# Optimization experiments

Hardware: AMD Instinct MI355X
Metric: run time of the kernel (lower is better)

The kernel has to match this reference:

```python
import jax, jax.numpy as jnp
import numpy as np

N_NODES = 50000
N_EDGES = 800000


def setup_inputs() -> dict:
    key = jax.random.key(0)
    ks = jax.random.split(key, 12)
    x = jax.random.normal(ks[0], (N_NODES, 500), dtype=jnp.float32)
    edge_src = jax.random.randint(ks[1], (N_EDGES,), 0, N_NODES, dtype=jnp.int32)
    edge_dst = jax.random.randint(ks[2], (N_EDGES,), 0, N_NODES, dtype=jnp.int32)
    edge_vals = jax.random.uniform(ks[3], (N_EDGES,), dtype=jnp.float32) * 0.1
    def w(k, fan_in, fan_out):
        s = 1.0 / np.sqrt(fan_in)
        return jax.random.uniform(k, (fan_in, fan_out), dtype=jnp.float32, minval=-s, maxval=s)
    W1 = w(ks[4], 500, 128)
    b1 = jnp.zeros((128,), jnp.float32)
    W2 = w(ks[5], 128, 64)
    b2 = jnp.zeros((64,), jnp.float32)
    W3 = w(ks[6], 64, 16)
    b3 = jnp.zeros((16,), jnp.float32)
    We = w(ks[7], 64, 64)
    be = jnp.zeros((64,), jnp.float32)
    return {"x": x, "edge_vals": edge_vals, "W1": W1, "b1": b1, "W2": W2,
            "b2": b2, "W3": W3, "b3": b3, "We": We, "be": be,
            "edge_src": edge_src, "edge_dst": edge_dst}


def reference(x, edge_vals, W1, b1, W2, b2, W3, b3, We, be, edge_src, edge_dst):
    n = x.shape[0]

    def gcn_layer(h, W, b):
        # GraphConvolution: support = h @ W ; out = spmm(adj, support) + b
        support = h @ W                                   # [N, d_out]
        msg = support[edge_dst] * edge_vals[:, None]      # [E, d_out]
        agg = jax.ops.segment_sum(msg, edge_src, num_segments=n)
        return agg + b

    h = jax.nn.relu(gcn_layer(x, W1, b1))
    # dropout omitted (eval mode, training=False)
    h = jax.nn.relu(gcn_layer(h, W2, b2))
    out1 = jax.nn.log_softmax(gcn_layer(h, W3, b3), axis=1)
    out2 = h @ We + be
    return (out1, out2)
```

## Files before the change

### kernel.cpp

```cpp
#include <hip/hip_runtime.h>
#include <math.h>

#define N_NODES 50000
#define N_EDGES 800000

typedef __attribute__((ext_vector_type(8))) short bf16x8;
typedef __attribute__((ext_vector_type(4))) float f32x4;

__device__ inline unsigned short f2bf(float f) {
    unsigned u = __float_as_uint(f);
    unsigned r = (u + 0x7fffu + ((u >> 16) & 1u)) >> 16;
    return (unsigned short)r;
}

__global__ __launch_bounds__(256) void convert_w1_kernel(
    const float* __restrict__ W1, unsigned short* __restrict__ W1bf)
{
    int t = blockIdx.x * 256 + threadIdx.x;
    int n = t >> 9, k = t & 511;
    float v = (k < 500) ? W1[k * 128 + n] : 0.0f;
    W1bf[t] = f2bf(v);
}

__global__ __launch_bounds__(256) void gemm1_mfma_kernel(
    const float* __restrict__ A,
    const unsigned short* __restrict__ Bt,
    unsigned short* __restrict__ C)
{
    constexpr int K = 500, N = 128, BM = 64;
    constexpr int LDA = 56;
    __shared__ __align__(16) unsigned short As[BM * LDA];

    const int t = threadIdx.x;
    const int row0 = blockIdx.x * BM;
    const int lane = t & 63;
    const int wave = t >> 6;
    const int wm = (wave & 1) * 32;
    const int wn = (wave >> 1) * 64;
    const int l15 = lane & 15;
    const int l4  = lane >> 4;

    const int m0 = t >> 3, kq = t & 7;
    const int m1 = m0 + 32;
    const float* arow0 = A + (size_t)(row0 + m0) * K;
    const float* arow1 = A + (size_t)(row0 + m1) * K;
    const bool rv0 = (row0 + m0) < N_NODES;
    const bool rv1 = (row0 + m1) < N_NODES;

    const f32x4 zero = {0.0f, 0.0f, 0.0f, 0.0f};
    f32x4 acc[2][4];
#pragma unroll
    for (int i = 0; i < 2; ++i)
#pragma unroll
        for (int j = 0; j < 4; ++j) acc[i][j] = zero;

    float4 pf0, pf1;
    auto ldA = [&](int k0, float4& d, const float* row, bool rowok) {
        int k = k0 + kq * 4;
        if (rowok && k < K) d = *reinterpret_cast<const float4*>(row + k);
        else d = make_float4(0.0f, 0.0f, 0.0f, 0.0f);
    };
    ldA(0, pf0, arow0, rv0);
    ldA(0, pf1, arow1, rv1);

    for (int s = 0; s < 16; ++s) {
        const int k0 = s * 32;
        __syncthreads();
        {
            unsigned short h[4];
            h[0] = f2bf(pf0.x); h[1] = f2bf(pf0.y);
            h[2] = f2bf(pf0.z); h[3] = f2bf(pf0.w);
            *reinterpret_cast<uint2*>(&As[m0 * LDA + kq * 4]) =
                *reinterpret_cast<uint2*>(h);
            h[0] = f2bf(pf1.x); h[1] = f2bf(pf1.y);
            h[2] = f2bf(pf1.z); h[3] = f2bf(pf1.w);
            *reinterpret_cast<uint2*>(&As[m1 * LDA + kq * 4]) =
                *reinterpret_cast<uint2*>(h);
        }
        __syncthreads();
        if (s < 15) {
            ldA(k0 + 32, pf0, arow0, rv0);
            ldA(k0 + 32, pf1, arow1, rv1);
        }

        bf16x8 af[2];
#pragma unroll
        for (int i = 0; i < 2; ++i) {
            int m = wm + i * 16 + l15;
            af[i] = *reinterpret_cast<const bf16x8*>(&As[m * LDA + l4 * 8]);
        }
        bf16x8 bfr[4];
#pragma unroll
        for (int j = 0; j < 4; ++j) {
            int n = wn + j * 16 + l15;
            bfr[j] = *reinterpret_cast<const bf16x8*>(
                Bt + (size_t)n * 512 + k0 + l4 * 8);
        }
#pragma unroll
        for (int i = 0; i < 2; ++i)
#pragma unroll
            for (int j = 0; j < 4; ++j)
                acc[i][j] = __builtin_amdgcn_mfma_f32_16x16x32_bf16(
                    af[i], bfr[j], acc[i][j], 0, 0, 0);
    }

#pragma unroll
    for (int i = 0; i < 2; ++i) {
#pragma unroll
        for (int r = 0; r < 4; ++r) {
            int row = row0 + wm + i * 16 + l4 * 4 + r;
            if (row < N_NODES) {
#pragma unroll
                for (int j = 0; j < 4; ++j) {
                    int col = wn + j * 16 + l15;
                    C[(size_t)row * N + col] = f2bf(acc[i][j][r]);
                }
            }
        }
    }
}

template <int K, int N, int TM, int TN, bool RELU_A, bool BIAS_C, bool OUT_BF16>
__global__ __launch_bounds__(256) void gemm_small_kernel(
    const float* __restrict__ A, const float* __restrict__ B,
    const float* __restrict__ bA, const float* __restrict__ bC,
    void* __restrict__ Cv, int M)
{
    constexpr int BM = 64;
    constexpr int BK = 32;
    constexpr int PAD = BM + 4;
    constexpr int RG = BM / TM;
    constexpr int CG = N / TN;
    static_assert(RG * CG == 256, "thread layout");
    static_assert(K % BK == 0, "K chunking");

    __shared__ float Bs[K * N];
    __shared__ float As[BK * PAD];

    const int t = threadIdx.x;
    const int row0 = blockIdx.x * BM;
    const int tx = t % CG;
    const int ty = t / CG;

    constexpr int BLOADS = (K * N) / 256;
#pragma unroll
    for (int i = 0; i < BLOADS; ++i) {
        int idx = t + i * 256;
        Bs[idx] = B[idx];
    }

    float acc[TM][TN] = {};

    for (int k0 = 0; k0 < K; k0 += BK) {
        float av[(BK * BM) / 256];
#pragma unroll
        for (int i = 0; i < (BK * BM) / 256; ++i) {
            int idx = t + i * 256;
            int kk = idx % BK, m = idx / BK;
            int gr = row0 + m;
            float v = (gr < M) ? A[(size_t)gr * K + k0 + kk] : 0.0f;
            if constexpr (RELU_A) {
                v += bA[k0 + kk];
                v = v > 0.0f ? v : 0.0f;
            }
            av[i] = v;
        }
        __syncthreads();
#pragma unroll
        for (int i = 0; i < (BK * BM) / 256; ++i) {
            int idx = t + i * 256;
            As[(idx % BK) * PAD + idx / BK] = av[i];
        }
        __syncthreads();
#pragma unroll
        for (int kk = 0; kk < BK; ++kk) {
            float a[TM], b[TN];
#pragma unroll
            for (int i = 0; i < TM; ++i) a[i] = As[kk * PAD + ty * TM + i];
#pragma unroll
            for (int j = 0; j < TN; ++j) b[j] = Bs[(k0 + kk) * N + tx * TN + j];
#pragma unroll
            for (int i = 0; i < TM; ++i)
#pragma unroll
                for (int j = 0; j < TN; ++j) acc[i][j] += a[i] * b[j];
        }
    }

#pragma unroll
    for (int i = 0; i < TM; ++i) {
        int gr = row0 + ty * TM + i;
        if (gr < M) {
            float v[TN];
#pragma unroll
            for (int j = 0; j < TN; ++j) {
                v[j] = acc[i][j];
                if constexpr (BIAS_C) v[j] += bC[tx * TN + j];
            }
            if constexpr (OUT_BF16) {
                unsigned short* C = (unsigned short*)Cv;
                if constexpr (TN == 4) {
                    unsigned short h[4] = {f2bf(v[0]), f2bf(v[1]), f2bf(v[2]), f2bf(v[3])};
                    *reinterpret_cast<uint2*>(C + (size_t)gr * N + tx * 4) =
                        *reinterpret_cast<uint2*>(h);
                } else {
#pragma unroll
                    for (int j = 0; j < TN; ++j)
                        C[(size_t)gr * N + tx * TN + j] = f2bf(v[j]);
                }
            } else {
                float* C = (float*)Cv;
                if constexpr (TN == 4) {
                    float4 q = {v[0], v[1], v[2], v[3]};
                    *reinterpret_cast<float4*>(C + (size_t)gr * N + tx * 4) = q;
                } else {
#pragma unroll
                    for (int j = 0; j < TN; ++j)
                        C[(size_t)gr * N + tx * TN + j] = v[j];
                }
            }
        }
    }
}

__global__ __launch_bounds__(256) void hist_kernel(
    const int* __restrict__ src, int* __restrict__ counts)
{
    int e = blockIdx.x * 256 + threadIdx.x;
    if (e < N_EDGES) atomicAdd(&counts[src[e]], 1);
}

__global__ __launch_bounds__(1024) void scan_kernel(
    const int* __restrict__ counts, int* __restrict__ row_ptr,
    int* __restrict__ cursor)
{
    constexpr int Q = N_NODES / 4;
    const int t = threadIdx.x;
    const int lane = t & 63, wave = t >> 6;
    __shared__ int wsum[16];
    __shared__ int carry_s;
    int carry = 0;
    const int4* c4 = reinterpret_cast<const int4*>(counts);
    int4* rp4 = reinterpret_cast<int4*>(row_ptr);
    int4* cu4 = reinterpret_cast<int4*>(cursor);

    for (int base = 0; base < Q; base += 1024) {
        const int g = base + t;
        int4 v = {0, 0, 0, 0};
        if (g < Q) v = c4[g];
        const int s = v.x + v.y + v.z + v.w;

        int incl = s;
#pragma unroll
        for (int off = 1; off < 64; off <<= 1) {
            int n = __shfl_up(incl, off, 64);
            if (lane >= off) incl += n;
        }
        if (lane == 63) wsum[wave] = incl;
        __syncthreads();
        if (t < 16) {
            int w = wsum[t];
            int inc = w;
#pragma unroll
            for (int off = 1; off < 16; off <<= 1) {
                int n = __shfl_up(inc, off, 64);
                if (t >= off) inc += n;
            }
            wsum[t] = inc - w;
            if (t == 15) carry_s = inc;
        }
        __syncthreads();
        if (g < Q) {
            int e0 = carry + wsum[wave] + (incl - s);
            int4 r;
            r.x = e0;
            r.y = r.x + v.x;
            r.z = r.y + v.y;
            r.w = r.z + v.z;
            rp4[g] = r;
            cu4[g] = r;
        }
        carry += carry_s;
        __syncthreads();
    }
    if (t == 0) row_ptr[N_NODES] = carry;
}

__global__ __launch_bounds__(256) void fill_kernel(
    const int* __restrict__ src, const int* __restrict__ dst,
    const float* __restrict__ vals, int* __restrict__ cursor,
    int2* __restrict__ pairs)
{
    int e = blockIdx.x * 256 + threadIdx.x;
    if (e >= N_EDGES) return;
    int pos = atomicAdd(&cursor[src[e]], 1);
    pairs[pos] = make_int2(dst[e], __float_as_int(vals[e]));
}

__global__ __launch_bounds__(256) void gather128_bf16_kernel(
    const unsigned short* __restrict__ support, const int2* __restrict__ pairs,
    const int* __restrict__ row_ptr, float* __restrict__ agg)
{
    const int node = blockIdx.x * 16 + (threadIdx.x >> 4);
    if (node >= N_NODES) return;
    const int lane = threadIdx.x & 15;
    int i = row_ptr[node];
    const int end = row_ptr[node + 1];

    float acc[8] = {};
    for (; i + 2 <= end; i += 2) {
        int2 p0 = pairs[i], p1 = pairs[i + 1];
        float v0 = __int_as_float(p0.y), v1 = __int_as_float(p1.y);
        uint4 r0 = *reinterpret_cast<const uint4*>(
            support + (size_t)p0.x * 128 + lane * 8);
        uint4 r1 = *reinterpret_cast<const uint4*>(
            support + (size_t)p1.x * 128 + lane * 8);
        unsigned w0[4] = {r0.x, r0.y, r0.z, r0.w};
        unsigned w1[4] = {r1.x, r1.y, r1.z, r1.w};
#pragma unroll
        for (int j = 0; j < 4; ++j) {
            acc[2 * j]     += __uint_as_float(w0[j] << 16) * v0;
            acc[2 * j + 1] += __uint_as_float(w0[j] & 0xffff0000u) * v0;
            acc[2 * j]     += __uint_as_float(w1[j] << 16) * v1;
            acc[2 * j + 1] += __uint_as_float(w1[j] & 0xffff0000u) * v1;
        }
    }
    if (i < end) {
        int2 p = pairs[i];
        float v = __int_as_float(p.y);
        uint4 r = *reinterpret_cast<const uint4*>(
            support + (size_t)p.x * 128 + lane * 8);
        unsigned w[4] = {r.x, r.y, r.z, r.w};
#pragma unroll
        for (int j = 0; j < 4; ++j) {
            acc[2 * j]     += __uint_as_float(w[j] << 16) * v;
            acc[2 * j + 1] += __uint_as_float(w[j] & 0xffff0000u) * v;
        }
    }
    float4 o0 = {acc[0], acc[1], acc[2], acc[3]};
    float4 o1 = {acc[4], acc[5], acc[6], acc[7]};
    float4* op = reinterpret_cast<float4*>(agg + (size_t)node * 128 + lane * 8);
    op[0] = o0; op[1] = o1;
}

__global__ __launch_bounds__(256) void gather64_bf16_kernel(
    const unsigned short* __restrict__ support, const int2* __restrict__ pairs,
    const int* __restrict__ row_ptr, float* __restrict__ agg)
{
    const int node = blockIdx.x * 32 + (threadIdx.x >> 3);
    if (node >= N_NODES) return;
    const int lane = threadIdx.x & 7;
    int i = row_ptr[node];
    const int end = row_ptr[node + 1];

    float acc[8] = {};
    for (; i + 2 <= end; i += 2) {
        int2 p0 = pairs[i], p1 = pairs[i + 1];
        float v0 = __int_as_float(p0.y), v1 = __int_as_float(p1.y);
        uint4 r0 = *reinterpret_cast<const uint4*>(
            support + (size_t)p0.x * 64 + lane * 8);
        uint4 r1 = *reinterpret_cast<const uint4*>(
            support + (size_t)p1.x * 64 + lane * 8);
        unsigned w0[4] = {r0.x, r0.y, r0.z, r0.w};
        unsigned w1[4] = {r1.x, r1.y, r1.z, r1.w};
#pragma unroll
        for (int j = 0; j < 4; ++j) {
            acc[2 * j]     += __uint_as_float(w0[j] << 16) * v0;
            acc[2 * j + 1] += __uint_as_float(w0[j] & 0xffff0000u) * v0;
            acc[2 * j]     += __uint_as_float(w1[j] << 16) * v1;
            acc[2 * j + 1] += __uint_as_float(w1[j] & 0xffff0000u) * v1;
        }
    }
    if (i < end) {
        int2 p = pairs[i];
        float v = __int_as_float(p.y);
        uint4 r = *reinterpret_cast<const uint4*>(
            support + (size_t)p.x * 64 + lane * 8);
        unsigned w[4] = {r.x, r.y, r.z, r.w};
#pragma unroll
        for (int j = 0; j < 4; ++j) {
            acc[2 * j]     += __uint_as_float(w[j] << 16) * v;
            acc[2 * j + 1] += __uint_as_float(w[j] & 0xffff0000u) * v;
        }
    }
    float4 o0 = {acc[0], acc[1], acc[2], acc[3]};
    float4 o1 = {acc[4], acc[5], acc[6], acc[7]};
    float4* op = reinterpret_cast<float4*>(agg + (size_t)node * 64 + lane * 8);
    op[0] = o0; op[1] = o1;
}

template <int F>
__global__ __launch_bounds__(256) void gather_kernel(
    const float* __restrict__ support, const int2* __restrict__ pairs,
    const int* __restrict__ row_ptr, float* __restrict__ agg)
{
    constexpr int TPN = F / 4;
    constexpr int NPB = 256 / TPN;
    const int node = blockIdx.x * NPB + threadIdx.x / TPN;
    if (node >= N_NODES) return;
    const int lane = threadIdx.x % TPN;
    int i = row_ptr[node];
    const int end = row_ptr[node + 1];

    float4 acc0 = {0, 0, 0, 0};
    float4 acc1 = {0, 0, 0, 0};

    for (; i + 2 <= end; i += 2) {
        int2 p0 = pairs[i];
        int2 p1 = pairs[i + 1];
        float v0 = __int_as_float(p0.y);
        float v1 = __int_as_float(p1.y);
        const float4 m0 = *reinterpret_cast<const float4*>(
            support + (size_t)p0.x * F + lane * 4);
        const float4 m1 = *reinterpret_cast<const float4*>(
            support + (size_t)p1.x * F + lane * 4);
        acc0.x += m0.x * v0; acc0.y += m0.y * v0;
        acc0.z += m0.z * v0; acc0.w += m0.w * v0;
        acc1.x += m1.x * v1; acc1.y += m1.y * v1;
        acc1.z += m1.z * v1; acc1.w += m1.w * v1;
    }
    if (i < end) {
        int2 p = pairs[i];
        float v = __int_as_float(p.y);
        const float4 m = *reinterpret_cast<const float4*>(
            support + (size_t)p.x * F + lane * 4);
        acc0.x += m.x * v; acc0.y += m.y * v;
        acc0.z += m.z * v; acc0.w += m.w * v;
    }
    acc0.x += acc1.x; acc0.y += acc1.y; acc0.z += acc1.z; acc0.w += acc1.w;
    *reinterpret_cast<float4*>(agg + (size_t)node * F + lane * 4) = acc0;
}

__global__ __launch_bounds__(256) void logsoftmax_kernel(
    const float* __restrict__ agg, const float* __restrict__ b3,
    float* __restrict__ out)
{
    int row = blockIdx.x * 256 + threadIdx.x;
    if (row >= N_NODES) return;
    float v[16];
    const float4* p = reinterpret_cast<const float4*>(agg + (size_t)row * 16);
#pragma unroll
    for (int i = 0; i < 4; ++i) {
        float4 q = p[i];
        v[i * 4 + 0] = q.x + b3[i * 4 + 0];
        v[i * 4 + 1] = q.y + b3[i * 4 + 1];
        v[i * 4 + 2] = q.z + b3[i * 4 + 2];
        v[i * 4 + 3] = q.w + b3[i * 4 + 3];
    }
    float mx = v[0];
#pragma unroll
    for (int i = 1; i < 16; ++i) mx = fmaxf(mx, v[i]);
    float s = 0.0f;
#pragma unroll
    for (int i = 0; i < 16; ++i) s += expf(v[i] - mx);
    float lse = mx + logf(s);
    float4* o = reinterpret_cast<float4*>(out + (size_t)row * 16);
#pragma unroll
    for (int i = 0; i < 4; ++i)
        o[i] = make_float4(v[i * 4 + 0] - lse, v[i * 4 + 1] - lse,
                           v[i * 4 + 2] - lse, v[i * 4 + 3] - lse);
}

extern "C" void kernel_launch(void* const* d_in, const int* in_sizes, int n_in,
                              void* d_out, int out_size, void* d_ws, size_t ws_size,
                              hipStream_t stream)
{
    const float* x         = (const float*)d_in[0];
    const float* edge_vals = (const float*)d_in[1];
    const float* W1 = (const float*)d_in[2];
    const float* b1 = (const float*)d_in[3];
    const float* W2 = (const float*)d_in[4];
    const float* b2 = (const float*)d_in[5];
    const float* W3 = (const float*)d_in[6];
    const float* b3 = (const float*)d_in[7];
    const float* We = (const float*)d_in[8];
    const float* be = (const float*)d_in[9];
    const int* esrc = (const int*)d_in[10];
    const int* edst = (const int*)d_in[11];

    float* out1 = (float*)d_out;
    float* out2 = (float*)d_out + (size_t)N_NODES * 16;

    char* ws = (char*)d_ws;
    float* bufA    = (float*)(ws);
    float* bufB    = (float*)(ws + 25600000);
    float* bufC    = (float*)(ws + 51200000);
    int*   counts  = (int*)  (ws + 54400000);
    int*   row_ptr = (int*)  (ws + 54600064);
    int*   cursor  = (int*)  (ws + 54800128);
    int2*  pairs   = (int2*) (ws + 55000192);

    unsigned short* W1bf   = (unsigned short*)bufC;
    unsigned short* sup1bf = (unsigned short*)bufA;
    unsigned short* sup2bf = (unsigned short*)bufA;

    const int MB = (N_NODES + 63) / 64;
    const int EB = (N_EDGES + 255) / 256;

    convert_w1_kernel<<<256, 256, 0, stream>>>(W1, W1bf);
    hipMemsetAsync(counts, 0, (size_t)N_NODES * 4, stream);
    hist_kernel<<<EB, 256, 0, stream>>>(esrc, counts);
    scan_kernel<<<1, 1024, 0, stream>>>(counts, row_ptr, cursor);
    fill_kernel<<<EB, 256, 0, stream>>>(esrc, edst, edge_vals, cursor, pairs);

    gemm1_mfma_kernel<<<MB, 256, 0, stream>>>(x, W1bf, sup1bf);

    gather128_bf16_kernel<<<(N_NODES + 15) / 16, 256, 0, stream>>>(
        sup1bf, pairs, row_ptr, bufB);

    gemm_small_kernel<128, 64, 4, 4, true, false, true><<<MB, 256, 0, stream>>>(
        bufB, W2, b1, nullptr, (void*)sup2bf, N_NODES);

    gather64_bf16_kernel<<<(N_NODES + 31) / 32, 256, 0, stream>>>(
        sup2bf, pairs, row_ptr, bufB);

    gemm_small_kernel<64, 64, 4, 4, true, true, false><<<MB, 256, 0, stream>>>(
        bufB, We, b2, be, (void*)out2, N_NODES);

    gemm_small_kernel<64, 16, 4, 1, true, false, false><<<MB, 256, 0, stream>>>(
        bufB, W3, b2, nullptr, (void*)bufA, N_NODES);

    gather_kernel<16><<<(N_NODES * 4 + 255) / 256, 256, 0, stream>>>(
        bufA, pairs, row_ptr, bufC);

    logsoftmax_kernel<<<(N_NODES + 255) / 256, 256, 0, stream>>>(bufC, b3, out1);
}
```

Before: 412.2 us.

## Move all dense GEMMs to wave-level bf16 MFMA and fuse bias/ReLU into gathers

Rewrites the first GEMM as a shared-memory-free, per-wave 16-row MFMA kernel. It replaces the scalar-FMA small GEMMs for W2 and for We/W3 with bf16 MFMA kernels, concatenating We and W3 into one weight matrix so a single pass produces both out2 and the layer-3 support. Bias and ReLU now run inside the gather kernels, which write bf16 hidden activations, cutting intermediate traffic and one extra GEMM launch. The cost is bf16 rounding of the hidden activations before the second and third layers, and uncoalesced per-lane global B loads with no LDS reuse.

Measured after the change: 417.1 us. No clear change (+1.2%).

```diff
diff --git a/kernel.cpp b/kernel.cpp
--- a/kernel.cpp
+++ b/kernel.cpp
@@ -13,13 +13,27 @@
     return (unsigned short)r;
 }
 
-__global__ __launch_bounds__(256) void convert_w1_kernel(
-    const float* __restrict__ W1, unsigned short* __restrict__ W1bf)
+__global__ __launch_bounds__(256) void convert_weights_kernel(
+    const float* __restrict__ W1, const float* __restrict__ W2,
+    const float* __restrict__ We, const float* __restrict__ W3,
+    unsigned short* __restrict__ W1bf, unsigned short* __restrict__ W2bf,
+    unsigned short* __restrict__ Wcat)
 {
     int t = blockIdx.x * 256 + threadIdx.x;
-    int n = t >> 9, k = t & 511;
-    float v = (k < 500) ? W1[k * 128 + n] : 0.0f;
-    W1bf[t] = f2bf(v);
+    if (t < 65536) {
+        int n = t >> 9, k = t & 511;
+        float v = (k < 500) ? W1[k * 128 + n] : 0.0f;
+        W1bf[t] = f2bf(v);
+    } else if (t < 65536 + 8192) {
+        int t2 = t - 65536;
+        int n = t2 >> 7, k = t2 & 127;
+        W2bf[t2] = f2bf(W2[k * 64 + n]);
+    } else if (t < 65536 + 8192 + 5120) {
+        int t3 = t - 65536 - 8192;
+        int n = t3 >> 6, k = t3 & 63;
+        float v = (n < 64) ? We[k * 64 + n] : W3[k * 16 + (n - 64)];
+        Wcat[t3] = f2bf(v);
+    }
 }
 
 __global__ __launch_bounds__(256) void gemm1_mfma_kernel(
@@ -27,197 +41,135 @@
     const unsigned short* __restrict__ Bt,
     unsigned short* __restrict__ C)
 {
-    constexpr int K = 500, N = 128, BM = 64;
-    constexpr int LDA = 56;
-    __shared__ __align__(16) unsigned short As[BM * LDA];
-
-    const int t = threadIdx.x;
-    const int row0 = blockIdx.x * BM;
-    const int lane = t & 63;
-    const int wave = t >> 6;
-    const int wm = (wave & 1) * 32;
-    const int wn = (wave >> 1) * 64;
-    const int l15 = lane & 15;
-    const int l4  = lane >> 4;
-
-    const int m0 = t >> 3, kq = t & 7;
-    const int m1 = m0 + 32;
-    const float* arow0 = A + (size_t)(row0 + m0) * K;
-    const float* arow1 = A + (size_t)(row0 + m1) * K;
-    const bool rv0 = (row0 + m0) < N_NODES;
-    const bool rv1 = (row0 + m1) < N_NODES;
+    const int wid  = (blockIdx.x * 256 + threadIdx.x) >> 6;
+    const int lane = threadIdx.x & 63;
+    const int r = lane & 15, q = lane >> 4;
+    const int row0 = wid * 16;
+    const int arow = row0 + r;
+    const bool valid = arow < N_NODES;
+    const float* ap = A + (size_t)arow * 500 + q * 8;
 
     const f32x4 zero = {0.0f, 0.0f, 0.0f, 0.0f};
-    f32x4 acc[2][4];
-#pragma unroll
-    for (int i = 0; i < 2; ++i)
-#pragma unroll
-        for (int j = 0; j < 4; ++j) acc[i][j] = zero;
-
-    float4 pf0, pf1;
-    auto ldA = [&](int k0, float4& d, const float* row, bool rowok) {
-        int k = k0 + kq * 4;
-        if (rowok && k < K) d = *reinterpret_cast<const float4*>(row + k);
-        else d = make_float4(0.0f, 0.0f, 0.0f, 0.0f);
-    };
-    ldA(0, pf0, arow0, rv0);
-    ldA(0, pf1, arow1, rv1);
-
+    f32x4 acc[8];
+#pragma unroll
+    for (int j = 0; j < 8; ++j) acc[j] = zero;
+
+#pragma unroll 4
     for (int s = 0; s < 16; ++s) {
-        const int k0 = s * 32;
-        __syncthreads();
-        {
-            unsigned short h[4];
-            h[0] = f2bf(pf0.x); h[1] = f2bf(pf0.y);
-            h[2] = f2bf(pf0.z); h[3] = f2bf(pf0.w);
-            *reinterpret_cast<uint2*>(&As[m0 * LDA + kq * 4]) =
-                *reinterpret_cast<uint2*>(h);
-            h[0] = f2bf(pf1.x); h[1] = f2bf(pf1.y);
-            h[2] = f2bf(pf1.z); h[3] = f2bf(pf1.w);
-            *reinterpret_cast<uint2*>(&As[m1 * LDA + kq * 4]) =
-                *reinterpret_cast<uint2*>(h);
-        }
-        __syncthreads();
-        if (s < 15) {
-            ldA(k0 + 32, pf0, arow0, rv0);
-            ldA(k0 + 32, pf1, arow1, rv1);
-        }
-
-        bf16x8 af[2];
-#pragma unroll
-        for (int i = 0; i < 2; ++i) {
-            int m = wm + i * 16 + l15;
-            af[i] = *reinterpret_cast<const bf16x8*>(&As[m * LDA + l4 * 8]);
-        }
-        bf16x8 bfr[4];
+        const int kb = s * 32 + q * 8;
+        float4 a0 = make_float4(0.f, 0.f, 0.f, 0.f);
+        float4 a1 = make_float4(0.f, 0.f, 0.f, 0.f);
+        if (valid && kb < 500)
+            a0 = *reinterpret_cast<const float4*>(ap + s * 32);
+        if (valid && kb + 4 < 500)
+            a1 = *reinterpret_cast<const float4*>(ap + s * 32 + 4);
+        unsigned short h[8] = {f2bf(a0.x), f2bf(a0.y), f2bf(a0.z), f2bf(a0.w),
+                               f2bf(a1.x), f2bf(a1.y), f2bf(a1.z), f2bf(a1.w)};
+        bf16x8 af = *reinterpret_cast<bf16x8*>(h);
+#pragma unroll
+        for (int j = 0; j < 8; ++j) {
+            bf16x8 bfr = *reinterpret_cast<const bf16x8*>(
+                Bt + (size_t)(j * 16 + r) * 512 + s * 32 + q * 8);
+            acc[j] = __builtin_amdgcn_mfma_f32_16x16x32_bf16(af, bfr, acc[j], 0, 0, 0);
+        }
+    }
+
+#pragma unroll
+    for (int reg = 0; reg < 4; ++reg) {
+        int grow = row0 + q * 4 + reg;
+        if (grow < N_NODES) {
+#pragma unroll
+            for (int j = 0; j < 8; ++j)
+                C[(size_t)grow * 128 + j * 16 + r] = f2bf(acc[j][reg]);
+        }
+    }
+}
+
+__global__ __launch_bounds__(256) void gemm2_mfma_kernel(
+    const unsigned short* __restrict__ A,
+    const unsigned short* __restrict__ Bt,
+    unsigned short* __restrict__ C)
+{
+    const int wid  = (blockIdx.x * 256 + threadIdx.x) >> 6;
+    const int lane = threadIdx.x & 63;
+    const int r = lane & 15, q = lane >> 4;
+    const int row0 = wid * 16;
+    const int arow = row0 + r;
+    const bool valid = arow < N_NODES;
+    const unsigned short* ap = A + (size_t)arow * 128 + q * 8;
+
+    const f32x4 zero = {0.0f, 0.0f, 0.0f, 0.0f};
+    f32x4 acc[4];
+#pragma unroll
+    for (int j = 0; j < 4; ++j) acc[j] = zero;
+
+#pragma unroll
+    for (int s = 0; s < 4; ++s) {
+        bf16x8 af = {};
+        if (valid) af = *reinterpret_cast<const bf16x8*>(ap + s * 32);
 #pragma unroll
         for (int j = 0; j < 4; ++j) {
-            int n = wn + j * 16 + l15;
-            bfr[j] = *reinterpret_cast<const bf16x8*>(
-                Bt + (size_t)n * 512 + k0 + l4 * 8);
-        }
-#pragma unroll
-        for (int i = 0; i < 2; ++i)
+            bf16x8 bfr = *reinterpret_cast<const bf16x8*>(
+                Bt + (size_t)(j * 16 + r) * 128 + s * 32 + q * 8);
+            acc[j] = __builtin_amdgcn_mfma_f32_16x16x32_bf16(af, bfr, acc[j], 0, 0, 0);
+        }
+    }
+
+#pragma unroll
+    for (int reg = 0; reg < 4; ++reg) {
+        int grow = row0 + q * 4 + reg;
+        if (grow < N_NODES) {
 #pragma unroll
             for (int j = 0; j < 4; ++j)
-                acc[i][j] = __builtin_amdgcn_mfma_f32_16x16x32_bf16(
-                    af[i], bfr[j], acc[i][j], 0, 0, 0);
-    }
-
-#pragma unroll
-    for (int i = 0; i < 2; ++i) {
-#pragma unroll
-        for (int r = 0; r < 4; ++r) {
-            int row = row0 + wm + i * 16 + l4 * 4 + r;
-            if (row < N_NODES) {
-#pragma unroll
-                for (int j = 0; j < 4; ++j) {
-                    int col = wn + j * 16 + l15;
-                    C[(size_t)row * N + col] = f2bf(acc[i][j][r]);
-                }
-            }
-        }
-    }
-}
-
-template <int K, int N, int TM, int TN, bool RELU_A, bool BIAS_C, bool OUT_BF16>
-__global__ __launch_bounds__(256) void gemm_small_kernel(
-    const float* __restrict__ A, const float* __restrict__ B,
-    const float* __restrict__ bA, const float* __restrict__ bC,
-    void* __restrict__ Cv, int M)
-{
-    constexpr int BM = 64;
-    constexpr int BK = 32;
-    constexpr int PAD = BM + 4;
-    constexpr int RG = BM / TM;
-    constexpr int CG = N / TN;
-    static_assert(RG * CG == 256, "thread layout");
-    static_assert(K % BK == 0, "K chunking");
-
-    __shared__ float Bs[K * N];
-    __shared__ float As[BK * PAD];
-
-    const int t = threadIdx.x;
-    const int row0 = blockIdx.x * BM;
-    const int tx = t % CG;
-    const int ty = t / CG;
-
-    constexpr int BLOADS = (K * N) / 256;
-#pragma unroll
-    for (int i = 0; i < BLOADS; ++i) {
-        int idx = t + i * 256;
-        Bs[idx] = B[idx];
-    }
-
-    float acc[TM][TN] = {};
-
-    for (int k0 = 0; k0 < K; k0 += BK) {
-        float av[(BK * BM) / 256];
-#pragma unroll
-        for (int i = 0; i < (BK * BM) / 256; ++i) {
-            int idx = t + i * 256;
-            int kk = idx % BK, m = idx / BK;
-            int gr = row0 + m;
-            float v = (gr < M) ? A[(size_t)gr * K + k0 + kk] : 0.0f;
-            if constexpr (RELU_A) {
-                v += bA[k0 + kk];
-                v = v > 0.0f ? v : 0.0f;
-            }
-            av[i] = v;
-        }
-        __syncthreads();
-#pragma unroll
-        for (int i = 0; i < (BK * BM) / 256; ++i) {
-            int idx = t + i * 256;
-            As[(idx % BK) * PAD + idx / BK] = av[i];
-        }
-        __syncthreads();
-#pragma unroll
-        for (int kk = 0; kk < BK; ++kk) {
-            float a[TM], b[TN];
-#pragma unroll
-            for (int i = 0; i < TM; ++i) a[i] = As[kk * PAD + ty * TM + i];
-#pragma unroll
-            for (int j = 0; j < TN; ++j) b[j] = Bs[(k0 + kk) * N + tx * TN + j];
-#pragma unroll
-            for (int i = 0; i < TM; ++i)
-#pragma unroll
-                for (int j = 0; j < TN; ++j) acc[i][j] += a[i] * b[j];
-        }
-    }
-
-#pragma unroll
-    for (int i = 0; i < TM; ++i) {
-        int gr = row0 + ty * TM + i;
-        if (gr < M) {
-            float v[TN];
-#pragma unroll
-            for (int j = 0; j < TN; ++j) {
-                v[j] = acc[i][j];
-                if constexpr (BIAS_C) v[j] += bC[tx * TN + j];
-            }
-            if constexpr (OUT_BF16) {
-                unsigned short* C = (unsigned short*)Cv;
-                if constexpr (TN == 4) {
-                    unsigned short h[4] = {f2bf(v[0]), f2bf(v[1]), f2bf(v[2]), f2bf(v[3])};
-                    *reinterpret_cast<uint2*>(C + (size_t)gr * N + tx * 4) =
-                        *reinterpret_cast<uint2*>(h);
-                } else {
-#pragma unroll
-                    for (int j = 0; j < TN; ++j)
-                        C[(size_t)gr * N + tx * TN + j] = f2bf(v[j]);
-                }
-            } else {
-                float* C = (float*)Cv;
-                if constexpr (TN == 4) {
-                    float4 q = {v[0], v[1], v[2], v[3]};
-                    *reinterpret_cast<float4*>(C + (size_t)gr * N + tx * 4) = q;
-                } else {
-#pragma unroll
-                    for (int j = 0; j < TN; ++j)
-                        C[(size_t)gr * N + tx * TN + j] = v[j];
-                }
-            }
+                C[(size_t)grow * 64 + j * 16 + r] = f2bf(acc[j][reg]);
+        }
+    }
+}
+
+__global__ __launch_bounds__(256) void gemm3_mfma_kernel(
+    const unsigned short* __restrict__ A,
+    const unsigned short* __restrict__ Bt,
+    const float* __restrict__ be,
+    float* __restrict__ out2,
+    float* __restrict__ sup3)
+{
+    const int wid  = (blockIdx.x * 256 + threadIdx.x) >> 6;
+    const int lane = threadIdx.x & 63;
+    const int r = lane & 15, q = lane >> 4;
+    const int row0 = wid * 16;
+    const int arow = row0 + r;
+    const bool valid = arow < N_NODES;
+    const unsigned short* ap = A + (size_t)arow * 64 + q * 8;
+
+    const f32x4 zero = {0.0f, 0.0f, 0.0f, 0.0f};
+    f32x4 acc[5];
+#pragma unroll
+    for (int j = 0; j < 5; ++j) acc[j] = zero;
+
+#pragma unroll
+    for (int s = 0; s < 2; ++s) {
+        bf16x8 af = {};
+        if (valid) af = *reinterpret_cast<const bf16x8*>(ap + s * 32);
+#pragma unroll
+        for (int j = 0; j < 5; ++j) {
+            bf16x8 bfr = *reinterpret_cast<const bf16x8*>(
+                Bt + (size_t)(j * 16 + r) * 64 + s * 32 + q * 8);
+            acc[j] = __builtin_amdgcn_mfma_f32_16x16x32_bf16(af, bfr, acc[j], 0, 0, 0);
+        }
+    }
+
+    float bev[4];
+#pragma unroll
+    for (int j = 0; j < 4; ++j) bev[j] = be[j * 16 + r];
+
+#pragma unroll
+    for (int reg = 0; reg < 4; ++reg) {
+        int grow = row0 + q * 4 + reg;
+        if (grow < N_NODES) {
+#pragma unroll
+            for (int j = 0; j < 4; ++j)
+                out2[(size_t)grow * 64 + j * 16 + r] = acc[j][reg] + bev[j];
+            sup3[(size_t)grow * 16 + r] = acc[4][reg];
         }
     }
 }
@@ -298,7 +250,8 @@
 
 __global__ __launch_bounds__(256) void gather128_bf16_kernel(
     const unsigned short* __restrict__ support, const int2* __restrict__ pairs,
-    const int* __restrict__ row_ptr, float* __restrict__ agg)
+    const int* __restrict__ row_ptr, const float* __restrict__ b1,
+    unsigned short* __restrict__ h1)
 {
     const int node = blockIdx.x * 16 + (threadIdx.x >> 4);
     if (node >= N_NODES) return;
@@ -336,15 +289,23 @@
             acc[2 * j + 1] += __uint_as_float(w[j] & 0xffff0000u) * v;
         }
     }
-    float4 o0 = {acc[0], acc[1], acc[2], acc[3]};
-    float4 o1 = {acc[4], acc[5], acc[6], acc[7]};
-    float4* op = reinterpret_cast<float4*>(agg + (size_t)node * 128 + lane * 8);
-    op[0] = o0; op[1] = o1;
+    const float4 ba = *reinterpret_cast<const float4*>(b1 + lane * 8);
+    const float4 bb = *reinterpret_cast<const float4*>(b1 + lane * 8 + 4);
+    float bias[8] = {ba.x, ba.y, ba.z, ba.w, bb.x, bb.y, bb.z, bb.w};
+    unsigned short h[8];
+#pragma unroll
+    for (int j = 0; j < 8; ++j) {
+        float v = acc[j] + bias[j];
+        h[j] = f2bf(v > 0.0f ? v : 0.0f);
+    }
+    *reinterpret_cast<uint4*>(h1 + (size_t)node * 128 + lane * 8) =
+        *reinterpret_cast<uint4*>(h);
 }
 
 __global__ __launch_bounds__(256) void gather64_bf16_kernel(
     const unsigned short* __restrict__ support, const int2* __restrict__ pairs,
-    const int* __restrict__ row_ptr, float* __restrict__ agg)
+    const int* __restrict__ row_ptr, const float* __restrict__ b2,
+    unsigned short* __restrict__ h2)
 {
     const int node = blockIdx.x * 32 + (threadIdx.x >> 3);
     if (node >= N_NODES) return;
@@ -382,22 +343,26 @@
             acc[2 * j + 1] += __uint_as_float(w[j] & 0xffff0000u) * v;
         }
     }
-    float4 o0 = {acc[0], acc[1], acc[2], acc[3]};
-    float4 o1 = {acc[4], acc[5], acc[6], acc[7]};
-    float4* op = reinterpret_cast<float4*>(agg + (size_t)node * 64 + lane * 8);
-    op[0] = o0; op[1] = o1;
-}
-
-template <int F>
-__global__ __launch_bounds__(256) void gather_kernel(
+    const float4 ba = *reinterpret_cast<const float4*>(b2 + lane * 8);
+    const float4 bb = *reinterpret_cast<const float4*>(b2 + lane * 8 + 4);
+    float bias[8] = {ba.x, ba.y, ba.z, ba.w, bb.x, bb.y, bb.z, bb.w};
+    unsigned short h[8];
+#pragma unroll
+    for (int j = 0; j < 8; ++j) {
+        float v = acc[j] + bias[j];
+        h[j] = f2bf(v > 0.0f ? v : 0.0f);
+    }
+    *reinterpret_cast<uint4*>(h2 + (size_t)node * 64 + lane * 8) =
+        *reinterpret_cast<uint4*>(h);
+}
+
+__global__ __launch_bounds__(256) void gather16_kernel(
     const float* __restrict__ support, const int2* __restrict__ pairs,
     const int* __restrict__ row_ptr, float* __restrict__ agg)
 {
-    constexpr int TPN = F / 4;
-    constexpr int NPB = 256 / TPN;
-    const int node = blockIdx.x * NPB + threadIdx.x / TPN;
+    const int node = blockIdx.x * 64 + (threadIdx.x >> 2);
     if (node >= N_NODES) return;
-    const int lane = threadIdx.x % TPN;
+    const int lane = threadIdx.x & 3;
     int i = row_ptr[node];
     const int end = row_ptr[node + 1];
 
@@ -410,9 +375,9 @@
         float v0 = __int_as_float(p0.y);
         float v1 = __int_as_float(p1.y);
         const float4 m0 = *reinterpret_cast<const float4*>(
-            support + (size_t)p0.x * F + lane * 4);
+            support + (size_t)p0.x * 16 + lane * 4);
         const float4 m1 = *reinterpret_cast<const float4*>(
-            support + (size_t)p1.x * F + lane * 4);
+            support + (size_t)p1.x * 16 + lane * 4);
         acc0.x += m0.x * v0; acc0.y += m0.y * v0;
         acc0.z += m0.z * v0; acc0.w += m0.w * v0;
         acc1.x += m1.x * v1; acc1.y += m1.y * v1;
@@ -422,12 +387,12 @@
         int2 p = pairs[i];
         float v = __int_as_float(p.y);
         const float4 m = *reinterpret_cast<const float4*>(
-            support + (size_t)p.x * F + lane * 4);
+            support + (size_t)p.x * 16 + lane * 4);
         acc0.x += m.x * v; acc0.y += m.y * v;
         acc0.z += m.z * v; acc0.w += m.w * v;
     }
     acc0.x += acc1.x; acc0.y += acc1.y; acc0.z += acc1.z; acc0.w += acc1.w;
-    *reinterpret_cast<float4*>(agg + (size_t)node * F + lane * 4) = acc0;
+    *reinterpret_cast<float4*>(agg + (size_t)node * 16 + lane * 4) = acc0;
 }
 
 __global__ __launch_bounds__(256) void logsoftmax_kernel(
@@ -489,38 +454,40 @@
     int*   cursor  = (int*)  (ws + 54800128);
     int2*  pairs   = (int2*) (ws + 55000192);
 
-    unsigned short* W1bf   = (unsigned short*)bufC;
+    unsigned short* W1bf = (unsigned short*)bufC;
+    unsigned short* W2bf = (unsigned short*)((char*)bufC + 131072);
+    unsigned short* Wcat = (unsigned short*)((char*)bufC + 147456);
+
     unsigned short* sup1bf = (unsigned short*)bufA;
+    unsigned short* h1bf   = (unsigned short*)bufB;
     unsigned short* sup2bf = (unsigned short*)bufA;
-
-    const int MB = (N_NODES + 63) / 64;
+    unsigned short* h2bf   = (unsigned short*)bufB;
+    float*          sup3   = bufA;
+    float*          agg3   = bufC;
+
+    const int WB = (N_NODES / 16 + 3) / 4;
     const int EB = (N_EDGES + 255) / 256;
 
-    convert_w1_kernel<<<256, 256, 0, stream>>>(W1, W1bf);
+    convert_weights_kernel<<<308, 256, 0, stream>>>(W1, W2, We, W3, W1bf, W2bf, Wcat);
     hipMemsetAsync(counts, 0, (size_t)N_NODES * 4, stream);
     hist_kernel<<<EB, 256, 0, stream>>>(esrc, counts);
     scan_kernel<<<1, 1024, 0, stream>>>(counts, row_ptr, cursor);
     fill_kernel<<<EB, 256, 0, stream>>>(esrc, edst, edge_vals, cursor, pairs);
 
-    gemm1_mfma_kernel<<<MB, 256, 0, stream>>>(x, W1bf, sup1bf);
+    gemm1_mfma_kernel<<<WB, 256, 0, stream>>>(x, W1bf, sup1bf);
 
     gather128_bf16_kernel<<<(N_NODES + 15) / 16, 256, 0, stream>>>(
-        sup1bf, pairs, row_ptr, bufB);
-
-    gemm_small_kernel<128, 64, 4, 4, true, false, true><<<MB, 256, 0, stream>>>(
-        bufB, W2, b1, nullptr, (void*)sup2bf, N_NODES);
+        sup1bf, pairs, row_ptr, b1, h1bf);
+
+    gemm2_mfma_kernel<<<WB, 256, 0, stream>>>(h1bf, W2bf, sup2bf);
 
     gather64_bf16_kernel<<<(N_NODES + 31) / 32, 256, 0, stream>>>(
-        sup2bf, pairs, row_ptr, bufB);
-
-    gemm_small_kernel<64, 64, 4, 4, true, true, false><<<MB, 256, 0, stream>>>(
-        bufB, We, b2, be, (void*)out2, N_NODES);
-
-    gemm_small_kernel<64, 16, 4, 1, true, false, false><<<MB, 256, 0, stream>>>(
-        bufB, W3, b2, nullptr, (void*)bufA, N_NODES);
-
-    gather_kernel<16><<<(N_NODES * 4 + 255) / 256, 256, 0, stream>>>(
-        bufA, pairs, row_ptr, bufC);
-
-    logsoftmax_kernel<<<(N_NODES + 255) / 256, 256, 0, stream>>>(bufC, b3, out1);
-}
+        sup2bf, pairs, row_ptr, b2, h2bf);
+
+    gemm3_mfma_kernel<<<WB, 256, 0, stream>>>(h2bf, Wcat, be, out2, sup3);
+
+    gather16_kernel<<<(N_NODES + 63) / 64, 256, 0, stream>>>(
+        sup3, pairs, row_ptr, agg3);
+
+    logsoftmax_kernel<<<(N_NODES + 255) / 256, 256, 0, stream>>>(agg3, b3, out1);
+}
```
